# Performance work log

Hardware: AMD Instinct MI355X
Metric: run time of the kernel (lower is better)

The kernel has to match this reference:

```python
import jax, jax.numpy as jnp
import numpy as np

BATCH, SEQ_LEN, INPUT_SIZE = 64, 4096, 64
RESERVOIR_SIZE = 128
SPECTRAL_RADIUS = 0.8
INPUT_SCALING = 0.3
LEAK_RATE = 0.5


def setup_inputs() -> dict:
    key = jax.random.key(0)
    k_x, k_in, k_res = jax.random.split(key, 3)
    input_seq = jax.random.normal(k_x, (BATCH, SEQ_LEN, INPUT_SIZE), dtype=jnp.float32)
    W_in = jax.random.normal(k_in, (RESERVOIR_SIZE, INPUT_SIZE), dtype=jnp.float32) * INPUT_SCALING
    W_res_np = np.asarray(jax.random.normal(k_res, (RESERVOIR_SIZE, RESERVOIR_SIZE), dtype=jnp.float32)) * 0.1
    spectral_rad = float(np.max(np.abs(np.linalg.eigvals(W_res_np))).real)
    if spectral_rad > 1e-06:
        W_res_np = W_res_np * (SPECTRAL_RADIUS / spectral_rad)
    W_res = jnp.asarray(W_res_np, dtype=jnp.float32)
    return {"input_seq": input_seq, "W_in": W_in, "W_res": W_res}


def reference(input_seq, W_in, W_res):
    # input_seq: [B, S, I]; W_in: [R, I]; W_res: [R, R]
    lr = LEAK_RATE
    # Precompute tanh(x_t @ W_in^T) for all t in one batched GEMM: [B, S, R]
    input_contrib = jnp.tanh(jnp.einsum('bsi,ri->bsr', input_seq, W_in))
    xs = jnp.transpose(input_contrib, (1, 0, 2))  # [S, B, R]

    def step(h, u_t):
        # h: [B, R]; u_t: [B, R]
        new_h = (1.0 - lr) * h + lr * jnp.tanh(u_t + h @ W_res.T)
        return new_h, new_h

    h0 = jnp.zeros((input_seq.shape[0], W_res.shape[0]), dtype=input_seq.dtype)
    _, states = jax.lax.scan(step, h0, xs)  # states: [S, B, R]
    return jnp.transpose(states, (1, 0, 2))  # [B, S, R]
```

## Files before the change

### kernel.cpp

```cpp
#include <hip/hip_runtime.h>

#define BATCH 64
#define SEQ   4096
#define ISZ   64
#define RSZ   128

typedef float  f32x4_t __attribute__((ext_vector_type(4)));
typedef __fp16 f16x2_t __attribute__((ext_vector_type(2)));

__device__ __forceinline__ float fast_tanh(float x) {
    float e = __expf(2.0f * x);
    return 1.0f - 2.0f / (e + 1.0f);
}

__device__ __forceinline__ float dot2(f16x2_t a, f16x2_t b, float c) {
#if __has_builtin(__builtin_amdgcn_fdot2)
    return __builtin_amdgcn_fdot2(a, b, c, false);
#else
    return fmaf((float)a.x, (float)b.x, fmaf((float)a.y, (float)b.y, c));
#endif
}

template <int CTRL>
__device__ __forceinline__ float dpp_add(float x) {
    int y = __builtin_amdgcn_update_dpp(0, __builtin_bit_cast(int, x),
                                        CTRL, 0xF, 0xF, true);
    return x + __builtin_bit_cast(float, y);
}

__global__ __launch_bounds__(256) void proj_kernel(
        const float* __restrict__ x, const float* __restrict__ w_in,
        float* __restrict__ out) {
    __shared__ float wT[ISZ][RSZ];
    __shared__ float xs[32][ISZ];

    const int tid = threadIdx.x;

    for (int idx = tid; idx < RSZ * ISZ / 4; idx += 256) {
        const int r  = idx >> 4;
        const int j4 = (idx & 15) << 2;
        const float4 v = reinterpret_cast<const float4*>(w_in)[idx];
        wT[j4 + 0][r] = v.x; wT[j4 + 1][r] = v.y;
        wT[j4 + 2][r] = v.z; wT[j4 + 3][r] = v.w;
    }
    const long row0 = (long)blockIdx.x * 32;
    #pragma unroll
    for (int q = 0; q < 2; ++q) {
        const int idx = tid + q * 256;
        reinterpret_cast<float4*>(&xs[0][0])[idx] =
            reinterpret_cast<const float4*>(x + row0 * ISZ)[idx];
    }
    __syncthreads();

    const int rq = tid & 31;
    const int rp = tid >> 5;
    const int r0 = rq << 2;
    const int ra = rp << 2;

    float acc[4][4] = {};
    #pragma unroll
    for (int j4 = 0; j4 < ISZ; j4 += 4) {
        float4 xv[4];
        #pragma unroll
        for (int m = 0; m < 4; ++m)
            xv[m] = *reinterpret_cast<const float4*>(&xs[ra + m][j4]);
        #pragma unroll
        for (int k = 0; k < 4; ++k) {
            const float4 w = *reinterpret_cast<const float4*>(&wT[j4 + k][r0]);
            #pragma unroll
            for (int m = 0; m < 4; ++m) {
                const float xm = k == 0 ? xv[m].x : k == 1 ? xv[m].y
                               : k == 2 ? xv[m].z : xv[m].w;
                acc[m][0] += xm * w.x; acc[m][1] += xm * w.y;
                acc[m][2] += xm * w.z; acc[m][3] += xm * w.w;
            }
        }
    }
    #pragma unroll
    for (int m = 0; m < 4; ++m) {
        float4 o;
        o.x = fast_tanh(acc[m][0]); o.y = fast_tanh(acc[m][1]);
        o.z = fast_tanh(acc[m][2]); o.w = fast_tanh(acc[m][3]);
        *reinterpret_cast<float4*>(&out[(row0 + ra + m) * RSZ + r0]) = o;
    }
}

__global__ __launch_bounds__(256) void scan_kernel(
        const float* __restrict__ w_res, float* __restrict__ io) {
    __shared__ float hq[2][80];
    __shared__ float stage[16 * 128];

    const int tid  = threadIdx.x;
    const int lane = tid & 63;
    const int wave = tid >> 6;
    const int grp  = lane >> 3;
    const int sl   = lane & 7;
    const int r0   = wave * 32 + grp * 4;
    const int kb   = sl * 16;

    f16x2_t w2[4][8];
    #pragma unroll
    for (int rr = 0; rr < 4; ++rr) {
        #pragma unroll
        for (int kk = 0; kk < 16; kk += 4) {
            const f32x4_t v = *reinterpret_cast<const f32x4_t*>(
                &w_res[(r0 + rr) * RSZ + kb + kk]);
            w2[rr][kk / 2]     = __builtin_amdgcn_cvt_pkrtz(v.x, v.y);
            w2[rr][kk / 2 + 1] = __builtin_amdgcn_cvt_pkrtz(v.z, v.w);
        }
    }

    for (int i = tid; i < 2 * 80; i += 256) (&hq[0][0])[i] = 0.0f;

    float* const out = io + (long)blockIdx.x * (SEQ * RSZ);
    const int hrd = 8 * sl;
    const int hwr = 16 * wave + 2 * grp;

    float4 u[4];
    #pragma unroll
    for (int s = 0; s < 4; ++s)
        u[s] = *reinterpret_cast<const float4*>(&out[s * RSZ + r0]);
    float4 hreg = {0.f, 0.f, 0.f, 0.f};
    __syncthreads();

    #define ACT(HH, VV)                                                       \
        (fmaf(0.5f, (HH), 0.5f) -                                             \
         __builtin_amdgcn_rcpf(                                               \
             __builtin_amdgcn_exp2f((VV) * 2.885390082f) + 1.0f))

    #define STEP(S)                                                           \
    {                                                                         \
        int tp = t0 + (S) + 4;                                                \
        if (tp > SEQ - 1) tp = SEQ - 1;                                       \
        const float4 uc = u[(S) & 3];                                         \
        u[(S) & 3] = *reinterpret_cast<const float4*>(&out[tp * RSZ + r0]);   \
        const float4 p0 = *reinterpret_cast<const float4*>(                   \
            &hq[(S) & 1][hrd]);                                               \
        const float4 p1 = *reinterpret_cast<const float4*>(                   \
            &hq[(S) & 1][hrd + 4]);                                           \
        f16x2_t hv[8];                                                        \
        hv[0] = __builtin_bit_cast(f16x2_t, p0.x);                            \
        hv[1] = __builtin_bit_cast(f16x2_t, p0.y);                            \
        hv[2] = __builtin_bit_cast(f16x2_t, p0.z);                            \
        hv[3] = __builtin_bit_cast(f16x2_t, p0.w);                            \
        hv[4] = __builtin_bit_cast(f16x2_t, p1.x);                            \
        hv[5] = __builtin_bit_cast(f16x2_t, p1.y);                            \
        hv[6] = __builtin_bit_cast(f16x2_t, p1.z);                            \
        hv[7] = __builtin_bit_cast(f16x2_t, p1.w);                            \
        float a0 = 0.f, a1 = 0.f, a2 = 0.f, a3 = 0.f;                         \
        _Pragma("unroll")                                                     \
        for (int j = 0; j < 8; ++j) {                                         \
            a0 = dot2(hv[j], w2[0][j], a0);                                   \
            a1 = dot2(hv[j], w2[1][j], a1);                                   \
            a2 = dot2(hv[j], w2[2][j], a2);                                   \
            a3 = dot2(hv[j], w2[3][j], a3);                                   \
        }                                                                     \
        a0 = dpp_add<0xB1>(a0);  a1 = dpp_add<0xB1>(a1);                      \
        a2 = dpp_add<0xB1>(a2);  a3 = dpp_add<0xB1>(a3);                      \
        a0 = dpp_add<0x4E>(a0);  a1 = dpp_add<0x4E>(a1);                      \
        a2 = dpp_add<0x4E>(a2);  a3 = dpp_add<0x4E>(a3);                      \
        a0 = dpp_add<0x141>(a0); a1 = dpp_add<0x141>(a1);                     \
        a2 = dpp_add<0x141>(a2); a3 = dpp_add<0x141>(a3);                     \
        float4 nh;                                                            \
        nh.x = ACT(hreg.x, uc.x + a0);                                        \
        nh.y = ACT(hreg.y, uc.y + a1);                                        \
        nh.z = ACT(hreg.z, uc.z + a2);                                        \
        nh.w = ACT(hreg.w, uc.w + a3);                                        \
        hreg = nh;                                                            \
        if (sl == 0) {                                                        \
            float2 pv;                                                        \
            pv.x = __builtin_bit_cast(float,                                  \
                       __builtin_amdgcn_cvt_pkrtz(nh.x, nh.y));               \
            pv.y = __builtin_bit_cast(float,                                  \
                       __builtin_amdgcn_cvt_pkrtz(nh.z, nh.w));               \
            *reinterpret_cast<float2*>(&hq[1 - ((S) & 1)][hwr]) = pv;         \
        } else if (sl == 1) {                                                 \
            *reinterpret_cast<float4*>(                                       \
                &stage[((t0 & 8) + (S)) * 128 + r0]) = nh;                    \
        }                                                                     \
        asm volatile("s_waitcnt lgkmcnt(0)" ::: "memory");                    \
        __builtin_amdgcn_s_barrier();                                         \
        asm volatile("" ::: "memory");                                        \
    }

    const int fstep = tid >> 5;
    const int felem = (tid & 31) * 4;

    for (int t0 = 0; t0 < SEQ; t0 += 8) {
        STEP(0) STEP(1) STEP(2) STEP(3)
        STEP(4) STEP(5) STEP(6) STEP(7)
        const f32x4_t v = *reinterpret_cast<const f32x4_t*>(
            &stage[((t0 & 8) + fstep) * 128 + felem]);
        __builtin_nontemporal_store(v,
            reinterpret_cast<f32x4_t*>(&out[(t0 + fstep) * RSZ + felem]));
    }
    #undef STEP
    #undef ACT
}

extern "C" void kernel_launch(void* const* d_in, const int* in_sizes, int n_in,
                              void* d_out, int out_size, void* d_ws, size_t ws_size,
                              hipStream_t stream) {
    const float* x     = (const float*)d_in[0];
    const float* w_in  = (const float*)d_in[1];
    const float* w_res = (const float*)d_in[2];
    float* out = (float*)d_out;

    proj_kernel<<<(BATCH * SEQ) / 32, 256, 0, stream>>>(x, w_in, out);
    scan_kernel<<<BATCH, 256, 0, stream>>>(w_res, out);
}
```

Baseline: 1.230 ms.

## Split scan dot-product chains and use packed FMA in input projection

In the recurrent scan step, the serial chain of 8 dependent dot2 accumulations per output is split into two independent 4-deep chains that are summed at the end. This shortens the per-timestep critical path on the latency-bound sequential scan. The input projection kernel is also rewritten to use 2-wide vector FMA on float2 accumulators, which may map to packed FP32 FMA instructions. The split adds one extra add per output and a few more registers, and slightly changes the floating-point summation order.

```diff
diff --git a/kernel.cpp b/kernel.cpp
--- a/kernel.cpp
+++ b/kernel.cpp
@@ -6,6 +6,7 @@
 #define RSZ   128
 
 typedef float  f32x4_t __attribute__((ext_vector_type(4)));
+typedef float  f32x2_t __attribute__((ext_vector_type(2)));
 typedef __fp16 f16x2_t __attribute__((ext_vector_type(2)));
 
 __device__ __forceinline__ float fast_tanh(float x) {
@@ -57,30 +58,33 @@
     const int r0 = rq << 2;
     const int ra = rp << 2;
 
-    float acc[4][4] = {};
+    f32x2_t acc[4][2] = {};
     #pragma unroll
     for (int j4 = 0; j4 < ISZ; j4 += 4) {
-        float4 xv[4];
+        f32x4_t xv[4];
         #pragma unroll
         for (int m = 0; m < 4; ++m)
-            xv[m] = *reinterpret_cast<const float4*>(&xs[ra + m][j4]);
+            xv[m] = *reinterpret_cast<const f32x4_t*>(&xs[ra + m][j4]);
         #pragma unroll
         for (int k = 0; k < 4; ++k) {
-            const float4 w = *reinterpret_cast<const float4*>(&wT[j4 + k][r0]);
+            const f32x4_t w = *reinterpret_cast<const f32x4_t*>(
+                &wT[j4 + k][r0]);
+            const f32x2_t w01 = w.xy, w23 = w.zw;
             #pragma unroll
             for (int m = 0; m < 4; ++m) {
                 const float xm = k == 0 ? xv[m].x : k == 1 ? xv[m].y
                                : k == 2 ? xv[m].z : xv[m].w;
-                acc[m][0] += xm * w.x; acc[m][1] += xm * w.y;
-                acc[m][2] += xm * w.z; acc[m][3] += xm * w.w;
+                f32x2_t xv2; xv2.x = xm; xv2.y = xm;
+                acc[m][0] = __builtin_elementwise_fma(xv2, w01, acc[m][0]);
+                acc[m][1] = __builtin_elementwise_fma(xv2, w23, acc[m][1]);
             }
         }
     }
     #pragma unroll
     for (int m = 0; m < 4; ++m) {
         float4 o;
-        o.x = fast_tanh(acc[m][0]); o.y = fast_tanh(acc[m][1]);
-        o.z = fast_tanh(acc[m][2]); o.w = fast_tanh(acc[m][3]);
+        o.x = fast_tanh(acc[m][0].x); o.y = fast_tanh(acc[m][0].y);
+        o.z = fast_tanh(acc[m][1].x); o.w = fast_tanh(acc[m][1].y);
         *reinterpret_cast<float4*>(&out[(row0 + ra + m) * RSZ + r0]) = o;
     }
 }
@@ -147,14 +151,20 @@
         hv[5] = __builtin_bit_cast(f16x2_t, p1.y);                            \
         hv[6] = __builtin_bit_cast(f16x2_t, p1.z);                            \
         hv[7] = __builtin_bit_cast(f16x2_t, p1.w);                            \
-        float a0 = 0.f, a1 = 0.f, a2 = 0.f, a3 = 0.f;                         \
+        float b0 = 0.f, b1 = 0.f, b2 = 0.f, b3 = 0.f;                         \
+        float c0 = 0.f, c1 = 0.f, c2 = 0.f, c3 = 0.f;                         \
         _Pragma("unroll")                                                     \
-        for (int j = 0; j < 8; ++j) {                                         \
-            a0 = dot2(hv[j], w2[0][j], a0);                                   \
-            a1 = dot2(hv[j], w2[1][j], a1);                                   \
-            a2 = dot2(hv[j], w2[2][j], a2);                                   \
-            a3 = dot2(hv[j], w2[3][j], a3);                                   \
+        for (int j = 0; j < 4; ++j) {                                         \
+            b0 = dot2(hv[j], w2[0][j], b0);                                   \
+            b1 = dot2(hv[j], w2[1][j], b1);                                   \
+            b2 = dot2(hv[j], w2[2][j], b2);                                   \
+            b3 = dot2(hv[j], w2[3][j], b3);                                   \
+            c0 = dot2(hv[j + 4], w2[0][j + 4], c0);                           \
+            c1 = dot2(hv[j + 4], w2[1][j + 4], c1);                           \
+            c2 = dot2(hv[j + 4], w2[2][j + 4], c2);                           \
+            c3 = dot2(hv[j + 4], w2[3][j + 4], c3);                           \
         }                                                                     \
+        float a0 = b0 + c0, a1 = b1 + c1, a2 = b2 + c2, a3 = b3 + c3;         \
         a0 = dpp_add<0xB1>(a0);  a1 = dpp_add<0xB1>(a1);                      \
         a2 = dpp_add<0xB1>(a2);  a3 = dpp_add<0xB1>(a3);                      \
         a0 = dpp_add<0x4E>(a0);  a1 = dpp_add<0x4E>(a1);                      \
```

New measurement: 1.288 ms. 1.05x slower.
